# Performance work log

Hardware: AMD Instinct MI355X
Metric: run time of the kernel (lower is better)

Reference implementation:

```python
import jax, jax.numpy as jnp
import numpy as np

N = 100000   # nodes
IN = 256     # in_dim
H = 64       # n_hid
A = 4        # n_adjs
E = 1600000  # nnz per adjacency
T = 4        # num node types
NC = 8       # classes
LN_EPS = 1e-5
RATIO = 1.0


def setup_inputs() -> dict:
    key = jax.random.key(0)
    ks = jax.random.split(key, 32)
    s = 0.02
    return {
        "node_feats": jax.random.normal(ks[0], (N, IN), jnp.float32),
        "node_types": jax.random.randint(ks[1], (N,), 0, T, jnp.int32),
        "adj_rows": jax.random.randint(ks[2], (A, E), 0, N, jnp.int32),
        "adj_cols": jax.random.randint(ks[3], (A, E), 0, N, jnp.int32),
        "adj_vals": jax.random.uniform(ks[4], (A, E), jnp.float32),
        "type_W": s * jax.random.normal(ks[5], (T, IN, H), jnp.float32),
        "type_b": s * jax.random.normal(ks[6], (T, H), jnp.float32),
        "affine_W0": s * jax.random.normal(ks[7], (H, H), jnp.float32),
        "affine_b0": s * jax.random.normal(ks[8], (H,), jnp.float32),
        "affine_W1": s * jax.random.normal(ks[9], (H, H), jnp.float32),
        "affine_b1": s * jax.random.normal(ks[10], (H,), jnp.float32),
        "as_seq0": 0.001 * jax.random.normal(ks[11], (2, A - 1), jnp.float32),
        "as_last_seq0": 0.001 * jax.random.normal(ks[12], (2,), jnp.float32),
        "as_res0": 0.001 * jax.random.normal(ks[13], (1, A), jnp.float32),
        "as_last_res0": 0.001 * jax.random.normal(ks[14], (2, 3), jnp.float32),
        "as_seq1": 0.001 * jax.random.normal(ks[15], (1, A - 1), jnp.float32),
        "as_last_seq1": 0.001 * jax.random.normal(ks[16], (2,), jnp.float32),
        "as_last_res1": 0.001 * jax.random.normal(ks[17], (1, 3), jnp.float32),
        "attn1_W": s * jax.random.normal(ks[18], (H, H), jnp.float32),
        "attn1_b": s * jax.random.normal(ks[19], (H,), jnp.float32),
        "attn2_W": s * jax.random.normal(ks[20], (H, 1), jnp.float32),
        "attn2_b": s * jax.random.normal(ks[21], (1,), jnp.float32),
        "cls_W": s * jax.random.normal(ks[22], (H, NC), jnp.float32),
        "cls_b": s * jax.random.normal(ks[23], (NC,), jnp.float32),
    }


def _spmm_all(rows, cols, vals, x):
    # for each of the A adjacencies: out[r] += v * x[c]  -> [A, N, H]
    def one(r, c, v):
        return jax.ops.segment_sum(v[:, None] * x[c], r, num_segments=x.shape[0])
    return jax.vmap(one)(rows, cols, vals)


def _op(S_sub, w):
    # Op with k=1: weighted sum over all candidate adjacencies, divided by count
    return jnp.einsum('a,anh->nh', w, S_sub) / S_sub.shape[0]


def _ln(x):
    m = x.mean(-1, keepdims=True)
    v = ((x - m) ** 2).mean(-1, keepdims=True)
    return (x - m) * jax.lax.rsqrt(v + LN_EPS)


def _forward(node_feats, node_types, adj_rows, adj_cols, adj_vals,
             type_W, type_b, affine_W0, affine_b0, affine_W1, affine_b1,
             as_seq0, as_last_seq0, as_res0, as_last_res0,
             as_seq1, as_last_seq1, as_last_res1,
             attn1_W, attn1_b, attn2_W, attn2_b, cls_W, cls_b):
    # per-node-type linear projection
    all_h = jnp.einsum('nd,tdh->tnh', node_feats, type_W)  # [T, N, H]
    hid = all_h[node_types, jnp.arange(node_feats.shape[0])] + type_b[node_types]

    w_seq0 = jax.nn.softmax(as_seq0, axis=-1)
    w_last_seq0 = jax.nn.softmax(as_last_seq0, axis=-1)
    w_res0 = jax.nn.softmax(as_res0, axis=-1)
    w_last_res0 = jax.nn.softmax(as_last_res0, axis=-1)
    w_seq1 = jax.nn.softmax(as_seq1, axis=-1)
    w_last_seq1 = jax.nn.softmax(as_last_seq1, axis=-1)
    w_last_res1 = jax.nn.softmax(as_last_res1, axis=-1)

    sub = jnp.array([0, 1, 3])  # cstr=[0,1] + last adjacency

    # ---- Cell 0 (n_step=3) ----
    x0 = hid @ affine_W0 + affine_b0
    S0 = _spmm_all(adj_rows, adj_cols, adj_vals, x0)
    s1 = _op(S0[:A - 1], w_seq0[0])                       # step 1 (res branch empty)
    S1 = _spmm_all(adj_rows, adj_cols, adj_vals, s1)
    s2 = _op(S1[:A - 1], w_seq0[1]) + RATIO * _op(S0, w_res0[0])
    S2 = _spmm_all(adj_rows, adj_cols, adj_vals, s2)
    out_seq = _op(S2[:2], w_last_seq0)                    # adjs_cstr = adjs[0],adjs[1]
    out_res = _op(S0[sub], w_last_res0[0]) + _op(S1[sub], w_last_res0[1])
    out0 = jax.nn.gelu(_ln(out_seq + RATIO * out_res), approximate=False)

    # ---- Cell 1 (n_step=2) ----
    x1 = hid @ affine_W1 + affine_b1
    T0 = _spmm_all(adj_rows, adj_cols, adj_vals, x1)
    t1 = _op(T0[:A - 1], w_seq1[0])
    T1 = _spmm_all(adj_rows, adj_cols, adj_vals, t1)
    out_seq1 = _op(T1[:2], w_last_seq1)
    out_res1 = _op(T0[sub], w_last_res1[0])
    out1 = jax.nn.gelu(_ln(out_seq1 + RATIO * out_res1), approximate=False)

    # ---- semantic attention over the two cells ----
    a0 = jnp.tanh(out0 @ attn1_W + attn1_b) @ attn2_W + attn2_b  # [N,1]
    a1 = jnp.tanh(out1 @ attn1_W + attn1_b) @ attn2_W + attn2_b
    attns = jax.nn.softmax(jnp.concatenate([a0, a1], axis=-1), axis=-1)  # [N,2]
    out = attns[:, 0:1] * out0 + attns[:, 1:2] * out1
    return out @ cls_W + cls_b  # [N, n_classes]


def reference(node_feats, node_types, adj_rows, adj_cols, adj_vals,
              type_W, type_b, affine_W0, affine_b0, affine_W1, affine_b1,
              as_seq0, as_last_seq0, as_res0, as_last_res0,
              as_seq1, as_last_seq1, as_last_res1,
              attn1_W, attn1_b, attn2_W, attn2_b, cls_W, cls_b):
    return _forward(node_feats, node_types, adj_rows, adj_cols, adj_vals,
                    type_W, type_b, affine_W0, affine_b0, affine_W1, affine_b1,
                    as_seq0, as_last_seq0, as_res0, as_last_res0,
                    as_seq1, as_last_seq1, as_last_res1,
                    attn1_W, attn1_b, attn2_W, attn2_b, cls_W, cls_b)
```

## Files before the change

### kernel.cpp

```cpp
#include <hip/hip_runtime.h>
#include <math.h>

#define NNODES 100000
#define NEDGE  1600000
#define HD     64
#define INDIM  256

#define RB   32
#define RBH  16
#define NB   3125
#define NKEY (4 * NB)
#define CAP  1024
#define CAPH 512
#define CHK  64
#define EPC  (NEDGE / CHK)
#define NCH  100
#define NPC  (NNODES / NCH)

static constexpr size_t NP = (size_t)NNODES * HD;
static constexpr size_t ME = (size_t)4 * NEDGE;
static constexpr int    M2 = NKEY * CHK;
static constexpr int    SCAN1B = (M2 + 1023) / 1024;

static constexpr size_t XPB_OFF   = 0;
static constexpr size_t SPB_OFF   = NP;
static constexpr size_t CRES_OFF  = 2 * NP;
static constexpr size_t CZ0_OFF   = 3 * NP;
static constexpr size_t CZ1_OFF   = 4 * NP;
static constexpr size_t S2B_OFF   = 5 * NP;
static constexpr size_t EPK_OFF   = 5 * NP + NP / 2;
static constexpr size_t CNT2_OFF  = EPK_OFF + 2 * ME;
static constexpr size_t OFF2_OFF  = CNT2_OFF + M2;
static constexpr size_t PART_OFF  = OFF2_OFF + M2;
static constexpr size_t OFF_OFF   = PART_OFF + 1024;
static constexpr size_t CNTK_OFF  = OFF_OFF + NKEY;
static constexpr size_t ROFF_OFF  = CNTK_OFF + NKEY;
static constexpr size_t NCNT_OFF  = ROFF_OFF + (size_t)NKEY * RB;
static constexpr size_t NOFF_OFF  = NCNT_OFF + 512;
static constexpr size_t NPERM_OFF = NOFF_OFF + 512;
static constexpr size_t WC_OFF    = NPERM_OFF + NNODES;

__device__ __forceinline__ float wave_bsum(float v) {
#pragma unroll
  for (int m = 1; m < 64; m <<= 1) v += __shfl_xor(v, m, 64);
  return v;
}

__device__ __forceinline__ unsigned int bf2pack(float a, float b) {
  unsigned int ua = __float_as_uint(a);
  ua += 0x7FFFu + ((ua >> 16) & 1u);
  unsigned int ub = __float_as_uint(b);
  ub += 0x7FFFu + ((ub >> 16) & 1u);
  return (ua >> 16) | (ub & 0xFFFF0000u);
}
__device__ __forceinline__ unsigned short bf1(float a) {
  unsigned int ua = __float_as_uint(a);
  ua += 0x7FFFu + ((ua >> 16) & 1u);
  return (unsigned short)(ua >> 16);
}
__device__ __forceinline__ float bf_lo(unsigned int g) { return __uint_as_float(g << 16); }
__device__ __forceinline__ float bf_hi(unsigned int g) { return __uint_as_float(g & 0xFFFF0000u); }
__device__ __forceinline__ float bf_s(unsigned short g) {
  return __uint_as_float((unsigned int)g << 16);
}
__device__ __forceinline__ float sload(const float* p) {
  return __uint_as_float(__builtin_amdgcn_readfirstlane(__float_as_uint(*p)));
}

__global__ void wcoef_kernel(const float* __restrict__ s0, const float* __restrict__ ls0,
                             const float* __restrict__ r0, const float* __restrict__ lr0,
                             const float* __restrict__ s1, const float* __restrict__ ls1,
                             const float* __restrict__ lr1, float* __restrict__ wc) {
  if (threadIdx.x != 0 || blockIdx.x != 0) return;
  auto sm2 = [](const float* a, float* o, float sc) {
    float m = fmaxf(a[0], a[1]);
    float e0 = expf(a[0] - m), e1 = expf(a[1] - m);
    float inv = sc / (e0 + e1);
    o[0] = e0 * inv; o[1] = e1 * inv;
  };
  auto sm3 = [](const float* a, float* o, float sc) {
    float m = fmaxf(a[0], fmaxf(a[1], a[2]));
    float e0 = expf(a[0] - m), e1 = expf(a[1] - m), e2 = expf(a[2] - m);
    float inv = sc / (e0 + e1 + e2);
    o[0] = e0 * inv; o[1] = e1 * inv; o[2] = e2 * inv;
  };
  auto sm4 = [](const float* a, float* o, float sc) {
    float m = fmaxf(fmaxf(a[0], a[1]), fmaxf(a[2], a[3]));
    float e0 = expf(a[0] - m), e1 = expf(a[1] - m), e2 = expf(a[2] - m), e3 = expf(a[3] - m);
    float inv = sc / (e0 + e1 + e2 + e3);
    o[0] = e0 * inv; o[1] = e1 * inv; o[2] = e2 * inv; o[3] = e3 * inv;
  };
  sm3(s0,      wc + 0,  1.f / 3.f);
  sm3(s0 + 3,  wc + 3,  1.f / 3.f);
  sm4(r0,      wc + 6,  0.25f);
  sm2(ls0,     wc + 10, 0.5f);
  sm3(lr0,     wc + 12, 1.f / 3.f);
  sm3(lr0 + 3, wc + 15, 1.f / 3.f);
  sm3(s1,      wc + 18, 1.f / 3.f);
  sm2(ls1,     wc + 21, 0.5f);
  sm3(lr1,     wc + 23, 1.f / 3.f);
}

__global__ __launch_bounds__(256) void nhist_kernel(const int* __restrict__ types,
                                                    int* __restrict__ ncnt) {
  __shared__ int c[4];
  int ch = blockIdx.x;
  if (threadIdx.x < 4) c[threadIdx.x] = 0;
  __syncthreads();
  int base = ch * NPC;
  for (int i = base + threadIdx.x; i < base + NPC; i += 256)
    atomicAdd(&c[types[i]], 1);
  __syncthreads();
  if (threadIdx.x < 4) ncnt[threadIdx.x * NCH + ch] = c[threadIdx.x];
}

__global__ __launch_bounds__(256) void nscan_kernel(const int* __restrict__ ncnt,
                                                    int* __restrict__ noff) {
  __shared__ int sdata[256];
  int t = threadIdx.x;
  int i0 = t * 2;
  int v0 = (i0 < 4 * NCH) ? ncnt[i0] : 0;
  int v1 = (i0 + 1 < 4 * NCH) ? ncnt[i0 + 1] : 0;
  int ts = v0 + v1;
  sdata[t] = ts;
  __syncthreads();
  for (int o = 1; o < 256; o <<= 1) {
    int x = (t >= o) ? sdata[t - o] : 0;
    __syncthreads();
    sdata[t] += x;
    __syncthreads();
  }
  int excl = sdata[t] - ts;
  if (i0 < 4 * NCH) noff[i0] = excl;
// ... 112 lines not shown
  if (t == 255) part[blockIdx.x] = sdata[255];
  if (base + 0 < M2) off2[base + 0] = excl;
  if (base + 1 < M2) off2[base + 1] = excl + v0;
  if (base + 2 < M2) off2[base + 2] = excl + v0 + v1;
  if (base + 3 < M2) off2[base + 3] = excl + v0 + v1 + v2;
}

__global__ __launch_bounds__(1024) void scan2_kernel(int* __restrict__ part) {
  __shared__ int sdata[1024];
  int t = threadIdx.x;
  int v = (t < SCAN1B) ? part[t] : 0;
  sdata[t] = v;
  __syncthreads();
  for (int o = 1; o < 1024; o <<= 1) {
    int x = (t >= o) ? sdata[t - o] : 0;
    __syncthreads();
    sdata[t] += x;
    __syncthreads();
  }
  if (t < SCAN1B) part[t] = sdata[t] - v;
}

__global__ __launch_bounds__(256) void scan3_kernel(int* __restrict__ off2,
                                                    const int* __restrict__ part) {
  int p = part[blockIdx.x];
  int t = threadIdx.x;
#pragma unroll
  for (int j = 0; j < 4; j++) {
    int i = blockIdx.x * 1024 + j * 256 + t;
    if (i < M2) off2[i] += p;
  }
}

__global__ __launch_bounds__(256) void keyoff_kernel(const int* __restrict__ off2,
                                                     int* __restrict__ off,
                                                     int* __restrict__ cntk) {
  int k = blockIdx.x * 256 + threadIdx.x;
  if (k >= NKEY) return;
  int s = off2[(size_t)k << 6];
  int e = (k + 1 < NKEY) ? off2[(size_t)(k + 1) << 6] : (int)ME;
  off[k] = s;
  cntk[k] = e - s;
}

__global__ __launch_bounds__(256) void scatterd_kernel(
    const int* __restrict__ rows, const int* __restrict__ cols, const float* __restrict__ vals,
    const int* __restrict__ off2, int2* __restrict__ epk) {
  __shared__ int cur[NB];
  int a = blockIdx.y, ch = blockIdx.x;
  for (int b = threadIdx.x; b < NB; b += 256)
    cur[b] = off2[((size_t)(a * NB + b) << 6) | ch];
  __syncthreads();
  int base = ch * EPC;
  for (int e = base + threadIdx.x; e < base + EPC; e += 256) {
    size_t idx = (size_t)a * NEDGE + e;
    int r = rows[idx];
    int pos = atomicAdd(&cur[r >> 5], 1);
    epk[pos] = make_int2(((r & 31) << 17) | cols[idx], __float_as_int(vals[idx]));
  }
}

__global__ __launch_bounds__(256) void pack_kernel(
    const int* __restrict__ off, const int* __restrict__ cnt,
    int2* __restrict__ epk, int* __restrict__ rofftab) {
  __shared__ int smeta[CAP];
  __shared__ float sval[CAP];
  __shared__ int h[RB], hc[RB];
  int key = blockIdx.x;
  int base = off[key], n = cnt[key];
  int t = threadIdx.x, wv = t >> 6, lane = t & 63;
  if (t < RB) h[t] = 0;
  __syncthreads();
  if (n <= CAP) {
    int lm[4]; float lv[4];
    int cl = 0;
#pragma unroll
    for (int j = 0; j < 4; j++) {
      int i = t + j * 256;
      if (i < n) {
        int2 p = epk[base + i];
        lm[cl] = p.x;
        lv[cl] = __int_as_float(p.y);
        cl++;
        atomicAdd(&h[p.x >> 17], 1);
      }
    }
    __syncthreads();
    if (wv == 0) {
      int v = (lane < RB) ? h[lane] : 0;
      int incl = v;
#pragma unroll
      for (int o = 1; o < RB; o <<= 1) {
        int x = __shfl_up(incl, o, 64);
        if (lane >= o) incl += x;
      }
      if (lane < RB) {
        int excl = incl - v;
        hc[lane] = excl;
        rofftab[(size_t)key * RB + lane] = excl;
      }
    }
    __syncthreads();
    for (int j = 0; j < cl; j++) {
      int p = atomicAdd(&hc[lm[j] >> 17], 1);
      smeta[p] = lm[j];
      sval[p] = lv[j];
    }
    __syncthreads();
    for (int i = t; i < n; i += 256)
      epk[base + i] = make_int2(smeta[i], __float_as_int(sval[i]));
  }
}


__global__ __launch_bounds__(256, 8) void st1_kernel(
    const int* __restrict__ off, const int* __restrict__ cnt,
    const int* __restrict__ rofftab, const int2* __restrict__ epk,
    const unsigned int* __restrict__ xpb, const float* __restrict__ wc,
    unsigned short* __restrict__ spb_s, unsigned short* __restrict__ spb_t,
    float* __restrict__ cres, float* __restrict__ cz0, float* __restrict__ cz1) {
  __shared__ int2 se[4 * CAPH];
  __shared__ int ro[4][RBH + 1];
  int bb = blockIdx.x;
  int b = bb >> 1, bh = bb & 1;
  int t = threadIdx.x, wv = t >> 6, lane = t & 63;
  float w_s1[4], w_res[4], w_z0[4], w_t1[4], w_z1[4];
#pragma unroll
  for (int a = 0; a < 4; a++) {
    w_s1[a]  = (a < 3) ? sload(wc + a) : 0.f;
    w_res[a] = sload(wc + 6 + a);
    w_z0[a]  = (a == 3) ? sload(wc + 14) : ((a < 2) ? sload(wc + 12 + a) : 0.f);
    w_t1[a]  = (a < 3) ? sload(wc + 18 + a) : 0.f;
    w_z1[a]  = (a == 3) ? sload(wc + 25) : ((a < 2) ? sload(wc + 23 + a) : 0.f);
  }
  int nA[4], baseA[4];
  bool fits = true;
#pragma unroll
  for (int a = 0; a < 4; a++) {
    int key = a * NB + b;
    int base = __builtin_amdgcn_readfirstlane(off[key]);
    int ntot = __builtin_amdgcn_readfirstlane(cnt[key]);
    int rs, re;
    if (ntot <= CAP) {
      int mid = __builtin_amdgcn_readfirstlane(rofftab[(size_t)key * RB + RBH]);
      rs = bh ? mid : 0;
      re = bh ? ntot : mid;
    } else {
      rs = 0; re = ntot; fits = false;
    }
    baseA[a] = base + rs;
    nA[a] = re - rs;
    if (nA[a] > CAPH) fits = false;
  }
  int rowbase = b * RB + bh * RBH + wv * 4;
  if (fits) {
#pragma unroll
    for (int a = 0; a < 4; a++) {
      int n = nA[a], base = baseA[a];
      for (int i = t; i < n; i += 256) {
        int2 p = epk[base + i];
        se[a * CAPH + i] = make_int2((p.x & 0x1FFFF) << 8, p.y);
      }
    }
    if (t < 4 * (RBH + 1)) {
      int a = t / (RBH + 1), rr = t % (RBH + 1);
      int key = a * NB + b;
      int rs0 = bh ? rofftab[(size_t)key * RB + RBH] : 0;
      int ar = bh * RBH + rr;
      int v = (ar < RB) ? rofftab[(size_t)key * RB + ar] : cnt[key];
      ro[a][rr] = v - rs0;
    }
    __syncthreads();
    const unsigned char* xb = (const unsigned char*)xpb;
    unsigned lane4 = (unsigned)lane << 2;
    auto tl2 = [&](const int2* sp, int i, int e, float& s0, float& s1,
                   float& t0, float& t1) {
      for (; i + 3 < e; i += 4) {
        int2 p0 = sp[i], p1 = sp[i + 1], p2 = sp[i + 2], p3 = sp[i + 3];
        unsigned g0 = *(const unsigned int*)(xb + ((unsigned)p0.x + lane4));
        unsigned g1 = *(const unsigned int*)(xb + ((unsigned)p1.x + lane4));
        unsigned g2 = *(const unsigned int*)(xb + ((unsigned)p2.x + lane4));
        unsigned g3 = *(const unsigned int*)(xb + ((unsigned)p3.x + lane4));
        float v0 = __int_as_float(p0.y), v1 = __int_as_float(p1.y);
        float v2 = __int_as_float(p2.y), v3 = __int_as_float(p3.y);
        s0 = fmaf(v0, bf_lo(g0), s0); t0 = fmaf(v0, bf_hi(g0), t0);
        s1 = fmaf(v1, bf_lo(g1), s1); t1 = fmaf(v1, bf_hi(g1), t1);
        s0 = fmaf(v2, bf_lo(g2), s0); t0 = fmaf(v2, bf_hi(g2), t0);
        s1 = fmaf(v3, bf_lo(g3), s1); t1 = fmaf(v3, bf_hi(g3), t1);
      }
      for (; i < e; i++) {
        int2 p = sp[i];
        unsigned g = *(const unsigned int*)(xb + ((unsigned)p.x + lane4));
        float v = __int_as_float(p.y);
        s0 = fmaf(v, bf_lo(g), s0); t0 = fmaf(v, bf_hi(g), t0);
      }
    };
    for (int r8 = 0; r8 < 4; r8++) {
      int r = wv * 4 + r8;
      float vs1 = 0.f, vt1 = 0.f, vres = 0.f, vz0 = 0.f, vz1 = 0.f;
#pragma unroll
      for (int ap = 0; ap < 2; ap++) {
        int aA = ap << 1, aB = aA | 1;
// ... 54 lines not shown
    for (int a = 0; a < 4; a++) {
      int base = baseA[a], n = nA[a];
      for (int i = 0; i < n; i++) {
        int2 p = epk[base + i];
        int lr = p.x >> 17, c = p.x & 0x1FFFF;
        float v = __int_as_float(p.y);
        unsigned int g = xpb[(size_t)c * 64 + lane];
        float gs = v * bf_lo(g), gt = v * bf_hi(g);
#pragma unroll
        for (int r8 = 0; r8 < 4; r8++) {
          if (lr == bh * RBH + wv * 4 + r8) {
            as1[r8]  = fmaf(w_s1[a], gs, as1[r8]);
            ares[r8] = fmaf(w_res[a], gs, ares[r8]);
            az0[r8]  = fmaf(w_z0[a], gs, az0[r8]);
            at1[r8]  = fmaf(w_t1[a], gt, at1[r8]);
            az1[r8]  = fmaf(w_z1[a], gt, az1[r8]);
          }
        }
      }
    }
#pragma unroll
    for (int r8 = 0; r8 < 4; r8++) {
      size_t o = (size_t)(rowbase + r8) * 64 + lane;
      spb_s[o] = bf1(as1[r8]);
      spb_t[o] = bf1(at1[r8]);
      cres[o] = ares[r8];
      cz0[o] = az0[r8];
      cz1[o] = az1[r8];
    }
  }
}

__global__ __launch_bounds__(256, 8) void st2_kernel(
    const int* __restrict__ off, const int* __restrict__ cnt,
    const int* __restrict__ rofftab, const int2* __restrict__ epk,
    const unsigned short* __restrict__ spb_s, const unsigned short* __restrict__ spb_t,
    const float* __restrict__ wc,
    const float* __restrict__ cres, unsigned short* __restrict__ s2b,
    float* __restrict__ cz0, float* __restrict__ cz1) {
  __shared__ int2 se[4 * CAPH];
  __shared__ int ro[4][RBH + 1];
  int bb = blockIdx.x;
  int b = bb >> 1, bh = bb & 1;
  int t = threadIdx.x, wv = t >> 6, lane = t & 63;
  float w_seq[4], w_z0[4], w_z1[4];
#pragma unroll
  for (int a = 0; a < 4; a++) {
    w_seq[a] = (a < 3) ? sload(wc + 3 + a) : 0.f;
    w_z0[a]  = (a == 3) ? sload(wc + 17) : ((a < 2) ? sload(wc + 15 + a) : 0.f);
    w_z1[a]  = (a < 2) ? sload(wc + 21 + a) : 0.f;
  }
  int nA[4], baseA[4];
  bool fits = true;
#pragma unroll
  for (int a = 0; a < 4; a++) {
    int key = a * NB + b;
    int base = __builtin_amdgcn_readfirstlane(off[key]);
    int ntot = __builtin_amdgcn_readfirstlane(cnt[key]);
    int rs, re;
    if (ntot <= CAP) {
      int mid = __builtin_amdgcn_readfirstlane(rofftab[(size_t)key * RB + RBH]);
      rs = bh ? mid : 0;
      re = bh ? ntot : mid;
    } else {
      rs = 0; re = ntot; fits = false;
    }
    baseA[a] = base + rs;
    nA[a] = re - rs;
    if (nA[a] > CAPH) fits = false;
  }
  int rowbase = b * RB + bh * RBH + wv * 4;
  if (fits) {
#pragma unroll
    for (int a = 0; a < 4; a++) {
      int n = nA[a], base = baseA[a];
      for (int i = t; i < n; i += 256) {
        int2 p = epk[base + i];
        se[a * CAPH + i] = make_int2((p.x & 0x1FFFF) << 7, p.y);
      }
    }
    if (t < 4 * (RBH + 1)) {
      int a = t / (RBH + 1), rr = t % (RBH + 1);
      int key = a * NB + b;
      int rs0 = bh ? rofftab[(size_t)key * RB + RBH] : 0;
      int ar = bh * RBH + rr;
      int v = (ar < RB) ? rofftab[(size_t)key * RB + ar] : cnt[key];
      ro[a][rr] = v - rs0;
    }
    __syncthreads();
    const unsigned char* sbs = (const unsigned char*)spb_s;
    const unsigned char* sbt = (const unsigned char*)spb_t;
    unsigned lane2 = (unsigned)lane << 1;
    auto tl2 = [&](const int2* sp, int i, int e, float& s0, float& s1,
                   float& t0, float& t1) {
      for (; i + 3 < e; i += 4) {
        int2 p0 = sp[i], p1 = sp[i + 1], p2 = sp[i + 2], p3 = sp[i + 3];
        float gs0 = bf_s(*(const unsigned short*)(sbs + ((unsigned)p0.x + lane2)));
        float gt0 = bf_s(*(const unsigned short*)(sbt + ((unsigned)p0.x + lane2)));
        float gs1 = bf_s(*(const unsigned short*)(sbs + ((unsigned)p1.x + lane2)));
        float gt1 = bf_s(*(const unsigned short*)(sbt + ((unsigned)p1.x + lane2)));
        float gs2 = bf_s(*(const unsigned short*)(sbs + ((unsigned)p2.x + lane2)));
        float gt2 = bf_s(*(const unsigned short*)(sbt + ((unsigned)p2.x + lane2)));
        float gs3 = bf_s(*(const unsigned short*)(sbs + ((unsigned)p3.x + lane2)));
        float gt3 = bf_s(*(const unsigned short*)(sbt + ((unsigned)p3.x + lane2)));
        float v0 = __int_as_float(p0.y), v1 = __int_as_float(p1.y);
        float v2 = __int_as_float(p2.y), v3 = __int_as_float(p3.y);
        s0 = fmaf(v0, gs0, s0); t0 = fmaf(v0, gt0, t0);
        s1 = fmaf(v1, gs1, s1); t1 = fmaf(v1, gt1, t1);
        s0 = fmaf(v2, gs2, s0); t0 = fmaf(v2, gt2, t0);
        s1 = fmaf(v3, gs3, s1); t1 = fmaf(v3, gt3, t1);
      }
      for (; i < e; i++) {
        int2 p = sp[i];
        float gs = bf_s(*(const unsigned short*)(sbs + ((unsigned)p.x + lane2)));
        float gt = bf_s(*(const unsigned short*)(sbt + ((unsigned)p.x + lane2)));
        float v = __int_as_float(p.y);
        s0 = fmaf(v, gs, s0); t0 = fmaf(v, gt, t0);
      }
    };
// ... 112 lines not shown
  } else {
    float dres[4], dz0[4], dz1[4];
#pragma unroll
    for (int r = 0; r < 4; r++) { dres[r] = 0.f; dz0[r] = 0.f; dz1[r] = 0.f; }
    for (int a = 0; a < 4; a++) {
      int base = baseA[a], n = nA[a];
      for (int i = 0; i < n; i++) {
        int2 p = epk[base + i];
        int lr = p.x >> 17, c = p.x & 0x1FFFF;
        float v = __int_as_float(p.y);
        float gs = v * bf_s(spb_s[(size_t)c * 64 + lane]);
        float gt = v * bf_s(spb_t[(size_t)c * 64 + lane]);
#pragma unroll
        for (int r8 = 0; r8 < 4; r8++) {
          if (lr == bh * RBH + wv * 4 + r8) {
            dres[r8] = fmaf(w_seq[a], gs, dres[r8]);
            dz0[r8]  = fmaf(w_z0[a], gs, dz0[r8]);
            dz1[r8]  = fmaf(w_z1[a], gt, dz1[r8]);
          }
        }
      }
    }
#pragma unroll
    for (int r8 = 0; r8 < 4; r8++) {
      size_t o = (size_t)(rowbase + r8) * 64 + lane;
      float s2v = cres[o] + dres[r8];
      s2b[o] = bf1(s2v);
      cz0[o] += dz0[r8];
      cz1[o] += dz1[r8];
    }
  }
}

__global__ __launch_bounds__(256, 8) void st3_kernel(
    const int* __restrict__ off, const int* __restrict__ cnt,
    const int* __restrict__ rofftab, const int2* __restrict__ epk,
    const unsigned short* __restrict__ s2b, const float* __restrict__ wc,
    float* __restrict__ cz0) {
  __shared__ int2 se[2 * CAPH];
  __shared__ int ro[2][RBH + 1];
  int bb = blockIdx.x;
  int b = bb >> 1, bh = bb & 1;
  int t = threadIdx.x, wv = t >> 6, lane = t & 63;
  float wA0 = sload(wc + 10), wA1 = sload(wc + 11);
  int nA[2], baseA[2];
  bool fits = true;
#pragma unroll
  for (int a = 0; a < 2; a++) {
    int key = a * NB + b;
    int base = __builtin_amdgcn_readfirstlane(off[key]);
    int ntot = __builtin_amdgcn_readfirstlane(cnt[key]);
    int rs, re;
    if (ntot <= CAP) {
      int mid = __builtin_amdgcn_readfirstlane(rofftab[(size_t)key * RB + RBH]);
      rs = bh ? mid : 0;
      re = bh ? ntot : mid;
    } else {
      rs = 0; re = ntot; fits = false;
    }
    baseA[a] = base + rs;
    nA[a] = re - rs;
    if (nA[a] > CAPH) fits = false;
  }
  int rowbase = b * RB + bh * RBH + wv * 4;
  if (fits) {
#pragma unroll
    for (int a = 0; a < 2; a++) {
      int n = nA[a], base = baseA[a];
      for (int i = t; i < n; i += 256) {
        int2 p = epk[base + i];
        se[a * CAPH + i] = make_int2((p.x & 0x1FFFF) << 7, p.y);
      }
    }
    if (t < 2 * (RBH + 1)) {
      int a = t / (RBH + 1), rr = t % (RBH + 1);
      int key = a * NB + b;
      int rs0 = bh ? rofftab[(size_t)key * RB + RBH] : 0;
      int ar = bh * RBH + rr;
      int v = (ar < RB) ? rofftab[(size_t)key * RB + ar] : cnt[key];
      ro[a][rr] = v - rs0;
    }
    __syncthreads();
    const unsigned char* sb = (const unsigned char*)s2b;
    unsigned lane2 = (unsigned)lane << 1;
    auto tlu = [&](const int2* sp, int i, int e, float& s0, float& s1) {
      for (; i + 3 < e; i += 4) {
        int2 p0 = sp[i], p1 = sp[i + 1], p2 = sp[i + 2], p3 = sp[i + 3];
        float g0 = bf_s(*(const unsigned short*)(sb + ((unsigned)p0.x + lane2)));
        float g1 = bf_s(*(const unsigned short*)(sb + ((unsigned)p1.x + lane2)));
        float g2 = bf_s(*(const unsigned short*)(sb + ((unsigned)p2.x + lane2)));
        float g3 = bf_s(*(const unsigned short*)(sb + ((unsigned)p3.x + lane2)));
        s0 = fmaf(__int_as_float(p0.y), g0, s0);
        s1 = fmaf(__int_as_float(p1.y), g1, s1);
        s0 = fmaf(__int_as_float(p2.y), g2, s0);
        s1 = fmaf(__int_as_float(p3.y), g3, s1);
      }
      for (; i < e; i++) {
        int2 p = sp[i];
        float g = bf_s(*(const unsigned short*)(sb + ((unsigned)p.x + lane2)));
        s0 = fmaf(__int_as_float(p.y), g, s0);
      }
    };
    for (int r8 = 0; r8 < 4; r8++) {
      int r = wv * 4 + r8;
      const int2* spA = se;
      const int2* spB = se + CAPH;
      int iA = ro[0][r], eA = ro[0][r + 1];
      int iB = ro[1][r], eB = ro[1][r + 1];
      float sA0 = 0.f, sA1 = 0.f, sB0 = 0.f, sB1 = 0.f;
      int dA = eA - iA, dB = eB - iB;
      int m = (dA < dB ? dA : dB) >> 2;
      for (int k = 0; k < m; k++) {
        int2 a0 = spA[iA], a1 = spA[iA + 1], a2 = spA[iA + 2], a3 = spA[iA + 3];
        int2 b0 = spB[iB], b1 = spB[iB + 1], b2 = spB[iB + 2], b3 = spB[iB + 3];
        float gA0 = bf_s(*(const unsigned short*)(sb + ((unsigned)a0.x + lane2)));
        float gA1 = bf_s(*(const unsigned short*)(sb + ((unsigned)a1.x + lane2)));
        float gA2 = bf_s(*(const unsigned short*)(sb + ((unsigned)a2.x + lane2)));
        float gA3 = bf_s(*(const unsigned short*)(sb + ((unsigned)a3.x + lane2)));
        float gB0 = bf_s(*(const unsigned short*)(sb + ((unsigned)b0.x + lane2)));
        float gB1 = bf_s(*(const unsigned short*)(sb + ((unsigned)b1.x + lane2)));
        float gB2 = bf_s(*(const unsigned short*)(sb + ((unsigned)b2.x + lane2)));
        float gB3 = bf_s(*(const unsigned short*)(sb + ((unsigned)b3.x + lane2)));
        sA0 = fmaf(__int_as_float(a0.y), gA0, sA0);
        sA1 = fmaf(__int_as_float(a1.y), gA1, sA1);
        sA0 = fmaf(__int_as_float(a2.y), gA2, sA0);
        sA1 = fmaf(__int_as_float(a3.y), gA3, sA1);
        sB0 = fmaf(__int_as_float(b0.y), gB0, sB0);
        sB1 = fmaf(__int_as_float(b1.y), gB1, sB1);
        sB0 = fmaf(__int_as_float(b2.y), gB2, sB0);
        sB1 = fmaf(__int_as_float(b3.y), gB3, sB1);
        iA += 4; iB += 4;
      }
      tlu(spA, iA, eA, sA0, sA1);
      tlu(spB, iB, eB, sB0, sB1);
      float vz = fmaf(wA0, sA0 + sA1, wA1 * (sB0 + sB1));
      size_t o = (size_t)(rowbase + r8) * 64 + lane;
      cz0[o] += vz;
    }
  } else {
    float dz[4];
#pragma unroll
    for (int r = 0; r < 4; r++) dz[r] = 0.f;
    for (int a = 0; a < 2; a++) {
      int base = baseA[a], n = nA[a];
      float wa = a ? wA1 : wA0;
      for (int i = 0; i < n; i++) {
        int2 p = epk[base + i];
        int lr = p.x >> 17, c = p.x & 0x1FFFF;
        float v = __int_as_float(p.y);
        float gs = v * bf_s(s2b[(size_t)c * 64 + lane]);
#pragma unroll
        for (int r8 = 0; r8 < 4; r8++) {
          if (lr == bh * RBH + wv * 4 + r8) dz[r8] = fmaf(wa, gs, dz[r8]);
        }
      }
    }
#pragma unroll
    for (int r8 = 0; r8 < 4; r8++) {
      size_t o = (size_t)(rowbase + r8) * 64 + lane;
      cz0[o] += dz[r8];
    }
  }
}

__global__ __launch_bounds__(256) void final_kernel(
    const float* __restrict__ cz0, const float* __restrict__ cz1,
    const float* __restrict__ attn1_W, const float* __restrict__ attn1_b,
    const float* __restrict__ attn2_W, const float* __restrict__ attn2_b,
    const float* __restrict__ cls_W, const float* __restrict__ cls_b,
    float* __restrict__ out) {
  int wave = threadIdx.x >> 6, lane = threadIdx.x & 63;
  int n = blockIdx.x * 4 + wave;
  if (n >= NNODES) return;
  size_t idx = (size_t)n * HD + lane;

  float z0 = cz0[idx];
  float z1 = cz1[idx];

  float m0 = wave_bsum(z0) * (1.f / 64.f);
  float dv0 = z0 - m0;
  float var0 = wave_bsum(dv0 * dv0) * (1.f / 64.f);
  float y0 = dv0 * rsqrtf(var0 + 1e-5f);
  float g0 = 0.5f * y0 * (1.f + erff(y0 * 0.70710678118654752f));

  float m1 = wave_bsum(z1) * (1.f / 64.f);
  float dv1 = z1 - m1;
  float var1 = wave_bsum(dv1 * dv1) * (1.f / 64.f);
  float y1 = dv1 * rsqrtf(var1 + 1e-5f);
  float g1 = 0.5f * y1 * (1.f + erff(y1 * 0.70710678118654752f));

  float t0 = attn1_b[lane], t1 = attn1_b[lane];
#pragma unroll 8
  for (int j = 0; j < 64; j++) {
    float w = attn1_W[j * HD + lane];
    t0 = fmaf(__shfl(g0, j, 64), w, t0);
    t1 = fmaf(__shfl(g1, j, 64), w, t1);
  }
  t0 = tanhf(t0);
  t1 = tanhf(t1);
  float aw = attn2_W[lane];
  float a0 = wave_bsum(t0 * aw) + attn2_b[0];
  float a1 = wave_bsum(t1 * aw) + attn2_b[0];
  float mx = fmaxf(a0, a1);
  float e0 = expf(a0 - mx), e1 = expf(a1 - mx);
  float inv = 1.f / (e0 + e1);
  float p0 = e0 * inv, p1 = e1 * inv;
  float o = p0 * g0 + p1 * g1;

#pragma unroll
  for (int k = 0; k < 8; k++) {
    float s = wave_bsum(o * cls_W[lane * 8 + k]);
    if (lane == k) out[(size_t)n * 8 + k] = s + cls_b[k];
  }
}

extern "C" void kernel_launch(void* const* d_in, const int* in_sizes, int n_in,
                              void* d_out, int out_size, void* d_ws, size_t ws_size,
                              hipStream_t stream) {
  const float* node_feats   = (const float*)d_in[0];
  const int*   node_types   = (const int*)d_in[1];
  const int*   adj_rows     = (const int*)d_in[2];
  const int*   adj_cols     = (const int*)d_in[3];
  const float* adj_vals     = (const float*)d_in[4];
  const float* type_W       = (const float*)d_in[5];
  const float* type_b       = (const float*)d_in[6];
  const float* aW0          = (const float*)d_in[7];
  const float* ab0          = (const float*)d_in[8];
  const float* aW1          = (const float*)d_in[9];
  const float* ab1          = (const float*)d_in[10];
  const float* as_seq0      = (const float*)d_in[11];
  const float* as_last_seq0 = (const float*)d_in[12];
  const float* as_res0      = (const float*)d_in[13];
  const float* as_last_res0 = (const float*)d_in[14];
  const float* as_seq1      = (const float*)d_in[15];
  const float* as_last_seq1 = (const float*)d_in[16];
  const float* as_last_res1 = (const float*)d_in[17];
  const float* attn1_W      = (const float*)d_in[18];
  const float* attn1_b      = (const float*)d_in[19];
  const float* attn2_W      = (const float*)d_in[20];
  const float* attn2_b      = (const float*)d_in[21];
  const float* cls_W        = (const float*)d_in[22];
  const float* cls_b        = (const float*)d_in[23];
  float* out = (float*)d_out;
  float* ws = (float*)d_ws;

  unsigned int*   xpb   = (unsigned int*)(ws + XPB_OFF);
  unsigned short* spb_s = (unsigned short*)(ws + SPB_OFF);
  unsigned short* spb_t = (unsigned short*)(ws + SPB_OFF + NP / 2);
  float*          cres  = ws + CRES_OFF;
  float*          cz0   = ws + CZ0_OFF;
  float*          cz1   = ws + CZ1_OFF;
  unsigned short* s2b   = (unsigned short*)(ws + S2B_OFF);
  int2*           epk   = (int2*)(ws + EPK_OFF);
  int*            cnt2  = (int*)(ws + CNT2_OFF);
  int*            off2  = (int*)(ws + OFF2_OFF);
  int*            part  = (int*)(ws + PART_OFF);
  int*            off   = (int*)(ws + OFF_OFF);
  int*            cntk  = (int*)(ws + CNTK_OFF);
  int*            roff  = (int*)(ws + ROFF_OFF);
  int*            ncnt  = (int*)(ws + NCNT_OFF);
  int*            noff  = (int*)(ws + NOFF_OFF);
  int*            nperm = (int*)(ws + NPERM_OFF);
  float*          wc    = ws + WC_OFF;

  wcoef_kernel<<<1, 64, 0, stream>>>(as_seq0, as_last_seq0, as_res0, as_last_res0,
                                     as_seq1, as_last_seq1, as_last_res1, wc);

  nhist_kernel<<<NCH, 256, 0, stream>>>(node_types, ncnt);
  nscan_kernel<<<1, 256, 0, stream>>>(ncnt, noff);
  nscatter_kernel<<<NCH, 256, 0, stream>>>(node_types, noff, nperm);
  hid2_kernel<<<NNODES / 32, 256, 0, stream>>>(node_feats, node_types, nperm,
                                               type_W, type_b, aW0, ab0, aW1, ab1, xpb);

  histb2_kernel<<<dim3(CHK, 4), 256, 0, stream>>>(adj_rows, cnt2);
  scan1_kernel<<<SCAN1B, 256, 0, stream>>>(cnt2, off2, part);
  scan2_kernel<<<1, 1024, 0, stream>>>(part);
  scan3_kernel<<<SCAN1B, 256, 0, stream>>>(off2, part);
  keyoff_kernel<<<(NKEY + 255) / 256, 256, 0, stream>>>(off2, off, cntk);
  scatterd_kernel<<<dim3(CHK, 4), 256, 0, stream>>>(adj_rows, adj_cols, adj_vals, off2, epk);
  pack_kernel<<<NKEY, 256, 0, stream>>>(off, cntk, epk, roff);

  st1_kernel<<<NB * 2, 256, 0, stream>>>(off, cntk, roff, epk, xpb, wc,
                                         spb_s, spb_t, cres, cz0, cz1);
  st2_kernel<<<NB * 2, 256, 0, stream>>>(off, cntk, roff, epk, spb_s, spb_t, wc,
                                         cres, s2b, cz0, cz1);
  st3_kernel<<<NB * 2, 256, 0, stream>>>(off, cntk, roff, epk, s2b, wc, cz0);

  final_kernel<<<NNODES / 4, 256, 0, stream>>>(cz0, cz1,
                                               attn1_W, attn1_b, attn2_W, attn2_b,
                                               cls_W, cls_b, out);
}
```

Baseline: 1.491 ms.

## Fuse final attention/classifier into st3 and drop wcoef/keyoff kernels

Removes the wcoef kernel by having each stage kernel compute its softmax mixing weights inline from the raw parameters. Removes the keyoff kernel by reading per-key base and count directly from the scanned off2 array. Fuses the final LayerNorm/GELU/attention/classifier epilogue into the st3 kernel, so cz0 is not written back and reread. This cuts three launches and one full pass over cz0/cz1, at the cost of more per-block work and register pressure in st3.

```diff
diff --git a/kernel.cpp b/kernel.cpp
--- a/kernel.cpp
+++ b/kernel.cpp
@@ -32,13 +32,10 @@
 static constexpr size_t CNT2_OFF  = EPK_OFF + 2 * ME;
 static constexpr size_t OFF2_OFF  = CNT2_OFF + M2;
 static constexpr size_t PART_OFF  = OFF2_OFF + M2;
-static constexpr size_t OFF_OFF   = PART_OFF + 1024;
-static constexpr size_t CNTK_OFF  = OFF_OFF + NKEY;
-static constexpr size_t ROFF_OFF  = CNTK_OFF + NKEY;
+static constexpr size_t ROFF_OFF  = PART_OFF + 1024;
 static constexpr size_t NCNT_OFF  = ROFF_OFF + (size_t)NKEY * RB;
 static constexpr size_t NOFF_OFF  = NCNT_OFF + 512;
 static constexpr size_t NPERM_OFF = NOFF_OFF + 512;
-static constexpr size_t WC_OFF    = NPERM_OFF + NNODES;
 
 __device__ __forceinline__ float wave_bsum(float v) {
 #pragma unroll
@@ -66,39 +63,23 @@
 __device__ __forceinline__ float sload(const float* p) {
   return __uint_as_float(__builtin_amdgcn_readfirstlane(__float_as_uint(*p)));
 }
-
-__global__ void wcoef_kernel(const float* __restrict__ s0, const float* __restrict__ ls0,
-                             const float* __restrict__ r0, const float* __restrict__ lr0,
-                             const float* __restrict__ s1, const float* __restrict__ ls1,
-                             const float* __restrict__ lr1, float* __restrict__ wc) {
-  if (threadIdx.x != 0 || blockIdx.x != 0) return;
-  auto sm2 = [](const float* a, float* o, float sc) {
-    float m = fmaxf(a[0], a[1]);
-    float e0 = expf(a[0] - m), e1 = expf(a[1] - m);
-    float inv = sc / (e0 + e1);
-    o[0] = e0 * inv; o[1] = e1 * inv;
-  };
-  auto sm3 = [](const float* a, float* o, float sc) {
-    float m = fmaxf(a[0], fmaxf(a[1], a[2]));
-    float e0 = expf(a[0] - m), e1 = expf(a[1] - m), e2 = expf(a[2] - m);
-    float inv = sc / (e0 + e1 + e2);
-    o[0] = e0 * inv; o[1] = e1 * inv; o[2] = e2 * inv;
-  };
-  auto sm4 = [](const float* a, float* o, float sc) {
-    float m = fmaxf(fmaxf(a[0], a[1]), fmaxf(a[2], a[3]));
-    float e0 = expf(a[0] - m), e1 = expf(a[1] - m), e2 = expf(a[2] - m), e3 = expf(a[3] - m);
-    float inv = sc / (e0 + e1 + e2 + e3);
-    o[0] = e0 * inv; o[1] = e1 * inv; o[2] = e2 * inv; o[3] = e3 * inv;
-  };
-  sm3(s0,      wc + 0,  1.f / 3.f);
-  sm3(s0 + 3,  wc + 3,  1.f / 3.f);
-  sm4(r0,      wc + 6,  0.25f);
-  sm2(ls0,     wc + 10, 0.5f);
-  sm3(lr0,     wc + 12, 1.f / 3.f);
-  sm3(lr0 + 3, wc + 15, 1.f / 3.f);
-  sm3(s1,      wc + 18, 1.f / 3.f);
-  sm2(ls1,     wc + 21, 0.5f);
-  sm3(lr1,     wc + 23, 1.f / 3.f);
+__device__ __forceinline__ void sm3d(float a0, float a1, float a2, float sc, float* o) {
+  float m = fmaxf(a0, fmaxf(a1, a2));
+  float e0 = expf(a0 - m), e1 = expf(a1 - m), e2 = expf(a2 - m);
+  float inv = sc / (e0 + e1 + e2);
+  o[0] = e0 * inv; o[1] = e1 * inv; o[2] = e2 * inv;
+}
+__device__ __forceinline__ void sm2d(float a0, float a1, float sc, float* o) {
+  float m = fmaxf(a0, a1);
+  float e0 = expf(a0 - m), e1 = expf(a1 - m);
+  float inv = sc / (e0 + e1);
+  o[0] = e0 * inv; o[1] = e1 * inv;
+}
+__device__ __forceinline__ void sm4d(float a0, float a1, float a2, float a3, float sc, float* o) {
+  float m = fmaxf(fmaxf(a0, a1), fmaxf(a2, a3));
+  float e0 = expf(a0 - m), e1 = expf(a1 - m), e2 = expf(a2 - m), e3 = expf(a3 - m);
+  float inv = sc / (e0 + e1 + e2 + e3);
+  o[0] = e0 * inv; o[1] = e1 * inv; o[2] = e2 * inv; o[3] = e3 * inv;
 }
 
 __global__ __launch_bounds__(256) void nhist_kernel(const int* __restrict__ types,
@@ -277,17 +258,6 @@
   }
 }
 
-__global__ __launch_bounds__(256) void keyoff_kernel(const int* __restrict__ off2,
-                                                     int* __restrict__ off,
-                                                     int* __restrict__ cntk) {
-  int k = blockIdx.x * 256 + threadIdx.x;
-  if (k >= NKEY) return;
-  int s = off2[(size_t)k << 6];
-  int e = (k + 1 < NKEY) ? off2[(size_t)(k + 1) << 6] : (int)ME;
-  off[k] = s;
-  cntk[k] = e - s;
-}
-
 __global__ __launch_bounds__(256) void scatterd_kernel(
     const int* __restrict__ rows, const int* __restrict__ cols, const float* __restrict__ vals,
     const int* __restrict__ off2, int2* __restrict__ epk) {
@@ -306,13 +276,15 @@
 }
 
 __global__ __launch_bounds__(256) void pack_kernel(
-    const int* __restrict__ off, const int* __restrict__ cnt,
+    const int* __restrict__ off2,
     int2* __restrict__ epk, int* __restrict__ rofftab) {
   __shared__ int smeta[CAP];
   __shared__ float sval[CAP];
   __shared__ int h[RB], hc[RB];
   int key = blockIdx.x;
-  int base = off[key], n = cnt[key];
+  int base = off2[(size_t)key << 6];
+  int kend = (key + 1 < NKEY) ? off2[(size_t)(key + 1) << 6] : (int)ME;
+  int n = kend - base;
   int t = threadIdx.x, wv = t >> 6, lane = t & 63;
   if (t < RB) h[t] = 0;
   __syncthreads();
@@ -358,10 +330,22 @@
 }
 
 
+__device__ __forceinline__ int key_base(const int* off2, int key) {
+  return __builtin_amdgcn_readfirstlane(off2[(size_t)key << 6]);
+}
+__device__ __forceinline__ int key_end(const int* off2, int key) {
+  return (key + 1 < NKEY)
+             ? __builtin_amdgcn_readfirstlane(off2[(size_t)(key + 1) << 6])
+             : (int)ME;
+}
+
 __global__ __launch_bounds__(256, 8) void st1_kernel(
-    const int* __restrict__ off, const int* __restrict__ cnt,
+    const int* __restrict__ off2,
     const int* __restrict__ rofftab, const int2* __restrict__ epk,
-    const unsigned int* __restrict__ xpb, const float* __restrict__ wc,
+    const unsigned int* __restrict__ xpb,
+    const float* __restrict__ as_seq0, const float* __restrict__ as_res0,
+    const float* __restrict__ as_last_res0, const float* __restrict__ as_seq1,
+    const float* __restrict__ as_last_res1,
     unsigned short* __restrict__ spb_s, unsigned short* __restrict__ spb_t,
     float* __restrict__ cres, float* __restrict__ cz0, float* __restrict__ cz1) {
   __shared__ int2 se[4 * CAPH];
@@ -369,22 +353,27 @@
   int bb = blockIdx.x;
   int b = bb >> 1, bh = bb & 1;
   int t = threadIdx.x, wv = t >> 6, lane = t & 63;
-  float w_s1[4], w_res[4], w_z0[4], w_t1[4], w_z1[4];
-#pragma unroll
-  for (int a = 0; a < 4; a++) {
-    w_s1[a]  = (a < 3) ? sload(wc + a) : 0.f;
-    w_res[a] = sload(wc + 6 + a);
-    w_z0[a]  = (a == 3) ? sload(wc + 14) : ((a < 2) ? sload(wc + 12 + a) : 0.f);
-    w_t1[a]  = (a < 3) ? sload(wc + 18 + a) : 0.f;
-    w_z1[a]  = (a == 3) ? sload(wc + 25) : ((a < 2) ? sload(wc + 23 + a) : 0.f);
-  }
+  float w_s1[4], w_res[4], w_z0[4], w_t1[4], w_z1[4], tmp[4];
+  sm3d(sload(as_seq0 + 0), sload(as_seq0 + 1), sload(as_seq0 + 2), 1.f / 3.f, tmp);
+  w_s1[0] = tmp[0]; w_s1[1] = tmp[1]; w_s1[2] = tmp[2]; w_s1[3] = 0.f;
+  sm4d(sload(as_res0 + 0), sload(as_res0 + 1), sload(as_res0 + 2), sload(as_res0 + 3),
+       0.25f, w_res);
+  sm3d(sload(as_last_res0 + 0), sload(as_last_res0 + 1), sload(as_last_res0 + 2),
+       1.f / 3.f, tmp);
+  w_z0[0] = tmp[0]; w_z0[1] = tmp[1]; w_z0[2] = 0.f; w_z0[3] = tmp[2];
+  sm3d(sload(as_seq1 + 0), sload(as_seq1 + 1), sload(as_seq1 + 2), 1.f / 3.f, tmp);
+  w_t1[0] = tmp[0]; w_t1[1] = tmp[1]; w_t1[2] = tmp[2]; w_t1[3] = 0.f;
+  sm3d(sload(as_last_res1 + 0), sload(as_last_res1 + 1), sload(as_last_res1 + 2),
+       1.f / 3.f, tmp);
+  w_z1[0] = tmp[0]; w_z1[1] = tmp[1]; w_z1[2] = 0.f; w_z1[3] = tmp[2];
+
   int nA[4], baseA[4];
   bool fits = true;
 #pragma unroll
   for (int a = 0; a < 4; a++) {
     int key = a * NB + b;
-    int base = __builtin_amdgcn_readfirstlane(off[key]);
-    int ntot = __builtin_amdgcn_readfirstlane(cnt[key]);
+    int base = key_base(off2, key);
+    int ntot = key_end(off2, key) - base;
     int rs, re;
     if (ntot <= CAP) {
       int mid = __builtin_amdgcn_readfirstlane(rofftab[(size_t)key * RB + RBH]);
@@ -410,9 +399,11 @@
     if (t < 4 * (RBH + 1)) {
       int a = t / (RBH + 1), rr = t % (RBH + 1);
       int key = a * NB + b;
+      int kb = off2[(size_t)key << 6];
+      int ke = (key + 1 < NKEY) ? off2[(size_t)(key + 1) << 6] : (int)ME;
       int rs0 = bh ? rofftab[(size_t)key * RB + RBH] : 0;
       int ar = bh * RBH + rr;
-      int v = (ar < RB) ? rofftab[(size_t)key * RB + ar] : cnt[key];
+      int v = (ar < RB) ? rofftab[(size_t)key * RB + ar] : (ke - kb);
       ro[a][rr] = v - rs0;
     }
     __syncthreads();
@@ -533,10 +524,11 @@
 }
 
 __global__ __launch_bounds__(256, 8) void st2_kernel(
-    const int* __restrict__ off, const int* __restrict__ cnt,
+    const int* __restrict__ off2,
     const int* __restrict__ rofftab, const int2* __restrict__ epk,
     const unsigned short* __restrict__ spb_s, const unsigned short* __restrict__ spb_t,
-    const float* __restrict__ wc,
+    const float* __restrict__ as_seq0, const float* __restrict__ as_last_res0,
+    const float* __restrict__ as_last_seq1,
     const float* __restrict__ cres, unsigned short* __restrict__ s2b,
     float* __restrict__ cz0, float* __restrict__ cz1) {
   __shared__ int2 se[4 * CAPH];
@@ -544,20 +536,22 @@
   int bb = blockIdx.x;
   int b = bb >> 1, bh = bb & 1;
   int t = threadIdx.x, wv = t >> 6, lane = t & 63;
-  float w_seq[4], w_z0[4], w_z1[4];
-#pragma unroll
-  for (int a = 0; a < 4; a++) {
-    w_seq[a] = (a < 3) ? sload(wc + 3 + a) : 0.f;
-    w_z0[a]  = (a == 3) ? sload(wc + 17) : ((a < 2) ? sload(wc + 15 + a) : 0.f);
-    w_z1[a]  = (a < 2) ? sload(wc + 21 + a) : 0.f;
-  }
+  float w_seq[4], w_z0[4], w_z1[4], tmp[4];
+  sm3d(sload(as_seq0 + 3), sload(as_seq0 + 4), sload(as_seq0 + 5), 1.f / 3.f, tmp);
+  w_seq[0] = tmp[0]; w_seq[1] = tmp[1]; w_seq[2] = tmp[2]; w_seq[3] = 0.f;
+  sm3d(sload(as_last_res0 + 3), sload(as_last_res0 + 4), sload(as_last_res0 + 5),
+       1.f / 3.f, tmp);
+  w_z0[0] = tmp[0]; w_z0[1] = tmp[1]; w_z0[2] = 0.f; w_z0[3] = tmp[2];
+  sm2d(sload(as_last_seq1 + 0), sload(as_last_seq1 + 1), 0.5f, tmp);
+  w_z1[0] = tmp[0]; w_z1[1] = tmp[1]; w_z1[2] = 0.f; w_z1[3] = 0.f;
+
   int nA[4], baseA[4];
   bool fits = true;
 #pragma unroll
   for (int a = 0; a < 4; a++) {
     int key = a * NB + b;
-    int base = __builtin_amdgcn_readfirstlane(off[key]);
-    int ntot = __builtin_amdgcn_readfirstlane(cnt[key]);
+    int base = key_base(off2, key);
+    int ntot = key_end(off2, key) - base;
     int rs, re;
     if (ntot <= CAP) {
       int mid = __builtin_amdgcn_readfirstlane(rofftab[(size_t)key * RB + RBH]);
@@ -583,9 +577,11 @@
     if (t < 4 * (RBH + 1)) {
       int a = t / (RBH + 1), rr = t % (RBH + 1);
       int key = a * NB + b;
+      int kb = off2[(size_t)key << 6];
+      int ke = (key + 1 < NKEY) ? off2[(size_t)(key + 1) << 6] : (int)ME;
       int rs0 = bh ? rofftab[(size_t)key * RB + RBH] : 0;
       int ar = bh * RBH + rr;
-      int v = (ar < RB) ? rofftab[(size_t)key * RB + ar] : cnt[key];
+      int v = (ar < RB) ? rofftab[(size_t)key * RB + ar] : (ke - kb);
       ro[a][rr] = v - rs0;
     }
     __syncthreads();
@@ -764,24 +760,30 @@
   }
 }
 
-__global__ __launch_bounds__(256, 8) void st3_kernel(
-    const int* __restrict__ off, const int* __restrict__ cnt,
+__global__ __launch_bounds__(256, 8) void st3f_kernel(
+    const int* __restrict__ off2,
     const int* __restrict__ rofftab, const int2* __restrict__ epk,
-    const unsigned short* __restrict__ s2b, const float* __restrict__ wc,
-    float* __restrict__ cz0) {
+    const unsigned short* __restrict__ s2b, const float* __restrict__ as_last_seq0,
+    const float* __restrict__ cz0, const float* __restrict__ cz1,
+    const float* __restrict__ attn1_W, const float* __restrict__ attn1_b,
+    const float* __restrict__ attn2_W, const float* __restrict__ attn2_b,
+    const float* __restrict__ cls_W, const float* __restrict__ cls_b,
+    float* __restrict__ out) {
   __shared__ int2 se[2 * CAPH];
   __shared__ int ro[2][RBH + 1];
   int bb = blockIdx.x;
   int b = bb >> 1, bh = bb & 1;
   int t = threadIdx.x, wv = t >> 6, lane = t & 63;
-  float wA0 = sload(wc + 10), wA1 = sload(wc + 11);
+  float wA[2];
+  sm2d(sload(as_last_seq0 + 0), sload(as_last_seq0 + 1), 0.5f, wA);
+  float wA0 = wA[0], wA1 = wA[1];
   int nA[2], baseA[2];
   bool fits = true;
 #pragma unroll
   for (int a = 0; a < 2; a++) {
     int key = a * NB + b;
-    int base = __builtin_amdgcn_readfirstlane(off[key]);
-    int ntot = __builtin_amdgcn_readfirstlane(cnt[key]);
+    int base = key_base(off2, key);
+    int ntot = key_end(off2, key) - base;
     int rs, re;
     if (ntot <= CAP) {
       int mid = __builtin_amdgcn_readfirstlane(rofftab[(size_t)key * RB + RBH]);
@@ -795,6 +797,9 @@
     if (nA[a] > CAPH) fits = false;
   }
   int rowbase = b * RB + bh * RBH + wv * 4;
+  float dz[4];
+#pragma unroll
+  for (int r = 0; r < 4; r++) dz[r] = 0.f;
   if (fits) {
 #pragma unroll
     for (int a = 0; a < 2; a++) {
@@ -807,9 +812,11 @@
     if (t < 2 * (RBH + 1)) {
       int a = t / (RBH + 1), rr = t % (RBH + 1);
       int key = a * NB + b;
+      int kb = off2[(size_t)key << 6];
+      int ke = (key + 1 < NKEY) ? off2[(size_t)(key + 1) << 6] : (int)ME;
       int rs0 = bh ? rofftab[(size_t)key * RB + RBH] : 0;
       int ar = bh * RBH + rr;
-      int v = (ar < RB) ? rofftab[(size_t)key * RB + ar] : cnt[key];
+      int v = (ar < RB) ? rofftab[(size_t)key * RB + ar] : (ke - kb);
       ro[a][rr] = v - rs0;
     }
     __syncthreads();
@@ -865,14 +872,9 @@
       }
       tlu(spA, iA, eA, sA0, sA1);
       tlu(spB, iB, eB, sB0, sB1);
-      float vz = fmaf(wA0, sA0 + sA1, wA1 * (sB0 + sB1));
-      size_t o = (size_t)(rowbase + r8) * 64 + lane;
-      cz0[o] += vz;
+      dz[r8] = fmaf(wA0, sA0 + sA1, wA1 * (sB0 + sB1));
     }
   } else {
-    float dz[4];
-#pragma unroll
-    for (int r = 0; r < 4; r++) dz[r] = 0.f;
     for (int a = 0; a < 2; a++) {
       int base = baseA[a], n = nA[a];
       float wa = a ? wA1 : wA0;
@@ -887,62 +889,50 @@
         }
       }
     }
-#pragma unroll
-    for (int r8 = 0; r8 < 4; r8++) {
-      size_t o = (size_t)(rowbase + r8) * 64 + lane;
-      cz0[o] += dz[r8];
-    }
-  }
-}
-
-__global__ __launch_bounds__(256) void final_kernel(
-    const float* __restrict__ cz0, const float* __restrict__ cz1,
-    const float* __restrict__ attn1_W, const float* __restrict__ attn1_b,
-    const float* __restrict__ attn2_W, const float* __restrict__ attn2_b,
-    const float* __restrict__ cls_W, const float* __restrict__ cls_b,
-    float* __restrict__ out) {
-  int wave = threadIdx.x >> 6, lane = threadIdx.x & 63;
-  int n = blockIdx.x * 4 + wave;
-  if (n >= NNODES) return;
-  size_t idx = (size_t)n * HD + lane;
-
-  float z0 = cz0[idx];
-  float z1 = cz1[idx];
-
-  float m0 = wave_bsum(z0) * (1.f / 64.f);
-  float dv0 = z0 - m0;
-  float var0 = wave_bsum(dv0 * dv0) * (1.f / 64.f);
-  float y0 = dv0 * rsqrtf(var0 + 1e-5f);
-  float g0 = 0.5f * y0 * (1.f + erff(y0 * 0.70710678118654752f));
-
-  float m1 = wave_bsum(z1) * (1.f / 64.f);
-  float dv1 = z1 - m1;
-  float var1 = wave_bsum(dv1 * dv1) * (1.f / 64.f);
-  float y1 = dv1 * rsqrtf(var1 + 1e-5f);
-  float g1 = 0.5f * y1 * (1.f + erff(y1 * 0.70710678118654752f));
-
-  float t0 = attn1_b[lane], t1 = attn1_b[lane];
+  }
+  float aw = attn2_W[lane];
+  float ab = attn1_b[lane];
+  float a2b = sload(attn2_b);
+  for (int r8 = 0; r8 < 4; r8++) {
+    size_t o = (size_t)(rowbase + r8) * 64 + lane;
+    float z0 = cz0[o] + dz[r8];
+    float z1 = cz1[o];
+
+    float m0 = wave_bsum(z0) * (1.f / 64.f);
+    float dv0 = z0 - m0;
+    float var0 = wave_bsum(dv0 * dv0) * (1.f / 64.f);
+    float y0 = dv0 * rsqrtf(var0 + 1e-5f);
+    float g0 = 0.5f * y0 * (1.f + erff(y0 * 0.70710678118654752f));
+
+    float m1 = wave_bsum(z1) * (1.f / 64.f);
+    float dv1 = z1 - m1;
+    float var1 = wave_bsum(dv1 * dv1) * (1.f / 64.f);
+    float y1 = dv1 * rsqrtf(var1 + 1e-5f);
+    float g1 = 0.5f * y1 * (1.f + erff(y1 * 0.70710678118654752f));
+
+    float t0 = ab, t1 = ab;
 #pragma unroll 8
-  for (int j = 0; j < 64; j++) {
-    float w = attn1_W[j * HD + lane];
-    t0 = fmaf(__shfl(g0, j, 64), w, t0);
-    t1 = fmaf(__shfl(g1, j, 64), w, t1);
-  }
-  t0 = tanhf(t0);
-  t1 = tanhf(t1);
-  float aw = attn2_W[lane];
-  float a0 = wave_bsum(t0 * aw) + attn2_b[0];
-  float a1 = wave_bsum(t1 * aw) + attn2_b[0];
-  float mx = fmaxf(a0, a1);
-  float e0 = expf(a0 - mx), e1 = expf(a1 - mx);
-  float inv = 1.f / (e0 + e1);
-  float p0 = e0 * inv, p1 = e1 * inv;
-  float o = p0 * g0 + p1 * g1;
-
-#pragma unroll
-  for (int k = 0; k < 8; k++) {
-    float s = wave_bsum(o * cls_W[lane * 8 + k]);
-    if (lane == k) out[(size_t)n * 8 + k] = s + cls_b[k];
+    for (int j = 0; j < 64; j++) {
+      float w = attn1_W[j * HD + lane];
+      t0 = fmaf(__shfl(g0, j, 64), w, t0);
+      t1 = fmaf(__shfl(g1, j, 64), w, t1);
+    }
+    t0 = tanhf(t0);
+    t1 = tanhf(t1);
+    float a0 = wave_bsum(t0 * aw) + a2b;
+    float a1 = wave_bsum(t1 * aw) + a2b;
+    float mx = fmaxf(a0, a1);
+    float e0 = expf(a0 - mx), e1 = expf(a1 - mx);
+    float inv = 1.f / (e0 + e1);
+    float p0 = e0 * inv, p1 = e1 * inv;
+    float ov = p0 * g0 + p1 * g1;
+
+    int n = rowbase + r8;
+#pragma unroll
+    for (int k = 0; k < 8; k++) {
+      float s = wave_bsum(ov * cls_W[lane * 8 + k]);
+      if (lane == k) out[(size_t)n * 8 + k] = s + cls_b[k];
+    }
   }
 }
 
@@ -987,16 +977,10 @@
   int*            cnt2  = (int*)(ws + CNT2_OFF);
   int*            off2  = (int*)(ws + OFF2_OFF);
   int*            part  = (int*)(ws + PART_OFF);
-  int*            off   = (int*)(ws + OFF_OFF);
-  int*            cntk  = (int*)(ws + CNTK_OFF);
   int*            roff  = (int*)(ws + ROFF_OFF);
   int*            ncnt  = (int*)(ws + NCNT_OFF);
   int*            noff  = (int*)(ws + NOFF_OFF);
   int*            nperm = (int*)(ws + NPERM_OFF);
-  float*          wc    = ws + WC_OFF;
-
-  wcoef_kernel<<<1, 64, 0, stream>>>(as_seq0, as_last_seq0, as_res0, as_last_res0,
-                                     as_seq1, as_last_seq1, as_last_res1, wc);
 
   nhist_kernel<<<NCH, 256, 0, stream>>>(node_types, ncnt);
   nscan_kernel<<<1, 256, 0, stream>>>(ncnt, noff);
@@ -1008,17 +992,18 @@
   scan1_kernel<<<SCAN1B, 256, 0, stream>>>(cnt2, off2, part);
   scan2_kernel<<<1, 1024, 0, stream>>>(part);
   scan3_kernel<<<SCAN1B, 256, 0, stream>>>(off2, part);
-  keyoff_kernel<<<(NKEY + 255) / 256, 256, 0, stream>>>(off2, off, cntk);
   scatterd_kernel<<<dim3(CHK, 4), 256, 0, stream>>>(adj_rows, adj_cols, adj_vals, off2, epk);
-  pack_kernel<<<NKEY, 256, 0, stream>>>(off, cntk, epk, roff);
-
-  st1_kernel<<<NB * 2, 256, 0, stream>>>(off, cntk, roff, epk, xpb, wc,
+  pack_kernel<<<NKEY, 256, 0, stream>>>(off2, epk, roff);
+
+  st1_kernel<<<NB * 2, 256, 0, stream>>>(off2, roff, epk, xpb,
+                                         as_seq0, as_res0, as_last_res0, as_seq1,
+                                         as_last_res1,
                                          spb_s, spb_t, cres, cz0, cz1);
-  st2_kernel<<<NB * 2, 256, 0, stream>>>(off, cntk, roff, epk, spb_s, spb_t, wc,
+  st2_kernel<<<NB * 2, 256, 0, stream>>>(off2, roff, epk, spb_s, spb_t,
+                                         as_seq0, as_last_res0, as_last_seq1,
                                          cres, s2b, cz0, cz1);
-  st3_kernel<<<NB * 2, 256, 0, stream>>>(off, cntk, roff, epk, s2b, wc, cz0);
-
-  final_kernel<<<NNODES / 4, 256, 0, stream>>>(cz0, cz1,
-                                               attn1_W, attn1_b, attn2_W, attn2_b,
-                                               cls_W, cls_b, out);
-}
+  st3f_kernel<<<NB * 2, 256, 0, stream>>>(off2, roff, epk, s2b, as_last_seq0,
+                                          cz0, cz1,
+                                          attn1_W, attn1_b, attn2_W, attn2_b,
+                                          cls_W, cls_b, out);
+}
```

Measured after the change: 1.447 ms. 1.03x faster.
